# Kernel tuning notes

Measured on AMD Instinct MI355X. Metric: run time of the kernel, lower is better.

Reference implementation:

```python
import jax, jax.numpy as jnp
import numpy as np

TEMP1, TEMP2, TEMP3 = 4.0, 5.0, 10.0  # forward() default temps
EPS = 1e-8


def setup_inputs() -> dict:
    key = jax.random.key(0)
    k1, k2 = jax.random.split(key)
    B, L, D = 64, 64, 512
    return {
        "ecg_embs": jax.random.normal(k1, (B, L, D), dtype=jnp.float32),
        "sent_embs": jax.random.normal(k2, (B, L, D), dtype=jnp.float32),
    }


def reference(ecg_embs, sent_embs):
    # Fully-batched version of the original per-sample Python loop.
    # i indexes the sentence (query) sample, j the ecg (context) sample.
    B, L, D = ecg_embs.shape
    # scores[i,j,s,q] = <ecg[j,s,:], sent[i,q,:]>  == contextT @ query in torch
    scores = jnp.einsum('jsd,iqd->ijsq', ecg_embs, sent_embs)
    # 1st softmax over query axis q
    attn = jax.nn.softmax(scores, axis=-1)
    # transpose to (i,j,q,s), temperature-scale, 2nd softmax over source axis s
    attn = jax.nn.softmax(TEMP1 * jnp.swapaxes(attn, -1, -2), axis=-1)  # (i,j,q,s)
    # weightedContext[i,j,q,:] = sum_s attn[i,j,q,s] * ecg[j,s,:]
    wctx = jnp.einsum('ijqs,jsd->ijqd', attn, ecg_embs)
    sent = sent_embs[:, None]  # (i,1,q,d) broadcast over j
    w12 = jnp.sum(sent * wctx, axis=-1)
    w1 = jnp.linalg.norm(sent, axis=-1)
    w2 = jnp.linalg.norm(wctx, axis=-1)
    cos = w12 / jnp.maximum(w1 * w2, EPS)  # (i,j,q)
    # row_sim.mul_(temp2).exp_().sum(dim=1).log() ; similarities[j,i] (cat along dim=1)
    sim = TEMP3 * jnp.log(jnp.sum(jnp.exp(TEMP2 * cos), axis=-1)).T  # (j,i)
    labels = jnp.arange(B)
    logp0 = jax.nn.log_softmax(sim, axis=-1)
    logp1 = jax.nn.log_softmax(sim.T, axis=-1)
    loss0 = -jnp.mean(logp0[labels, labels])
    loss1 = -jnp.mean(logp1[labels, labels])
    # att_maps: list of attn[i] from iteration i == diagonal (i==j) attention,
    # each shaped (1, queryL, ih=1, iw=sourceL); stacked -> (B, 1, L, 1, L)
    att_maps = attn[labels, labels][:, None, :, None, :]
    return (loss0 + loss1) / 2.0, att_maps
```

## Files before the change

### kernel.cpp

```cpp
#include <hip/hip_runtime.h>
#include <math.h>

typedef __attribute__((ext_vector_type(8))) short short8;
typedef __attribute__((ext_vector_type(4))) float f32x4;
typedef __attribute__((ext_vector_type(16))) float f32x16;
typedef unsigned int uint;
typedef unsigned short ushort;

#define T1 4.0f
#define T2 5.0f
#define T3 10.0f
#define EPSF 1e-8f
#define SST 68

__device__ inline ushort f2bf(float x) {
    union { float f; uint u; } a; a.f = x;
    uint r = a.u + 0x7FFFu + ((a.u >> 16) & 1u);
    return (ushort)(r >> 16);
}
__device__ inline float bf2f(ushort h) {
    union { uint u; float f; } a; a.u = ((uint)h) << 16;
    return a.f;
}

#define GLDS(gsrc, ldst) \
    __builtin_amdgcn_global_load_lds( \
        (const __attribute__((address_space(1))) uint*)(gsrc), \
        (__attribute__((address_space(3))) uint*)(ldst), 16, 0, 0)

__global__ __launch_bounds__(256) void prep_kernel(
        const float* __restrict__ ecg, const float* __restrict__ sent,
        char* __restrict__ EH, char* __restrict__ EL,
        char* __restrict__ SH, char* __restrict__ SL,
        char* __restrict__ Gp, float* __restrict__ w1) {
    __shared__ float partial[256];
    const int bid = blockIdx.x;
    const int tensor = bid >> 6, idx = bid & 63;
    const float* src = (tensor ? sent : ecg) + (size_t)idx * 32768;
    char* dh = (tensor ? SH : EH) + (size_t)idx * 65536;
    char* dl = (tensor ? SL : EL) + (size_t)idx * 65536;
    const int tid = threadIdx.x;
    const int r = tid & 63;
    float s2 = 0.f;
    #pragma unroll
    for (int it = 0; it < 4; it++) {
        int kc = it * 4 + (tid >> 6);
        const float* p = src + r * 512 + kc * 32;
        char* oh = dh + kc * 4096 + r * 64;
        char* ol = dl + kc * 4096 + r * 64;
        #pragma unroll
        for (int c = 0; c < 4; c++) {
            float4 v0 = *(const float4*)(p + c * 8);
            float4 v1 = *(const float4*)(p + c * 8 + 4);
            float x[8] = {v0.x, v0.y, v0.z, v0.w, v1.x, v1.y, v1.z, v1.w};
            uint hw[4], lw[4];
            #pragma unroll
            for (int e = 0; e < 4; e++) {
                float a0 = x[2 * e], a1 = x[2 * e + 1];
                ushort h0 = f2bf(a0), h1 = f2bf(a1);
                hw[e] = (uint)h0 | ((uint)h1 << 16);
                ushort l0 = f2bf(a0 - bf2f(h0)), l1 = f2bf(a1 - bf2f(h1));
                lw[e] = (uint)l0 | ((uint)l1 << 16);
                s2 += a0 * a0 + a1 * a1;
            }
            int phys = (c + (r >> 1)) & 3;
            uint4 H; H.x = hw[0]; H.y = hw[1]; H.z = hw[2]; H.w = hw[3];
            *(uint4*)(oh + phys * 16) = H;
            uint4 L; L.x = lw[0]; L.y = lw[1]; L.z = lw[2]; L.w = lw[3];
            *(uint4*)(ol + phys * 16) = L;
        }
    }
    partial[tid] = s2;
    __syncthreads();
    if (tensor == 1) {
        if (tid < 64) {
            float t = partial[tid] + partial[tid + 64] + partial[tid + 128] + partial[tid + 192];
            w1[idx * 64 + tid] = sqrtf(t);
        }
        return;
    }

    {
        const char* srcH = EH + (size_t)idx * 65536;
        const char* srcL = EL + (size_t)idx * 65536;
        const int wv = tid >> 6, lane = tid & 63;
        const int wq = wv >> 1, wn = wv & 1;
        const int quad = lane >> 4, ln = lane & 15;

        int ao[2], bo[2];
        #pragma unroll
        for (int mi = 0; mi < 2; mi++) {
            int R = 32 * wq + 16 * mi + ln;
            ao[mi] = R * 64 + ((quad + (R >> 1)) & 3) * 16;
        }
        #pragma unroll
        for (int ni = 0; ni < 2; ni++) {
            int R = 32 * wn + 16 * ni + ln;
            bo[ni] = R * 64 + ((quad + (R >> 1)) & 3) * 16;
        }

        f32x4 acc[2][2];
        #pragma unroll
        for (int a = 0; a < 2; a++)
            #pragma unroll
            for (int b = 0; b < 2; b++) acc[a][b] = (f32x4){0.f, 0.f, 0.f, 0.f};

        #pragma unroll 2
        for (int kc = 0; kc < 16; kc++) {
            const char* ph = srcH + (size_t)kc * 4096;
            const char* pl = srcL + (size_t)kc * 4096;
            short8 ah[2], al[2], bh[2], bl[2];
            #pragma unroll
            for (int mi = 0; mi < 2; mi++) {
                ah[mi] = *(const short8*)(ph + ao[mi]);
                al[mi] = *(const short8*)(pl + ao[mi]);
            }
            #pragma unroll
            for (int ni = 0; ni < 2; ni++) {
                bh[ni] = *(const short8*)(ph + bo[ni]);
                bl[ni] = *(const short8*)(pl + bo[ni]);
            }
            #pragma unroll
            for (int mi = 0; mi < 2; mi++)
                #pragma unroll
                for (int ni = 0; ni < 2; ni++) {
                    acc[mi][ni] = __builtin_amdgcn_mfma_f32_16x16x32_bf16(ah[mi], bh[ni], acc[mi][ni], 0, 0, 0);
                    acc[mi][ni] = __builtin_amdgcn_mfma_f32_16x16x32_bf16(ah[mi], bl[ni], acc[mi][ni], 0, 0, 0);
                    acc[mi][ni] = __builtin_amdgcn_mfma_f32_16x16x32_bf16(al[mi], bh[ni], acc[mi][ni], 0, 0, 0);
                }
        }
        #pragma unroll
        for (int mi = 0; mi < 2; mi++)
            #pragma unroll
            for (int ni = 0; ni < 2; ni++)
                #pragma unroll
                for (int rr = 0; rr < 4; rr++) {
                    int t = 32 * wq + 16 * mi + quad * 4 + rr;
                    int u = 32 * wn + 16 * ni + ln;
                    float g = acc[mi][ni][rr];
                    ushort h = f2bf(g);
                    ushort l = f2bf(g - bf2f(h));
                    char* base = Gp + (size_t)idx * 16384 + t * 128 + (((u >> 3) + t) & 7) * 16 + (u & 7) * 2;
                    *(ushort*)base = h;
                    *(ushort*)(base + 8192) = l;
                }
    }
}

__global__ __launch_bounds__(256, 4) void pair_kernel(
        const char* __restrict__ EH, const char* __restrict__ EL,
        const char* __restrict__ SH, const char* __restrict__ SL,
        const char* __restrict__ Gp, const float* __restrict__ w1g,
        float* __restrict__ simval, float* __restrict__ out) {

    __shared__ __align__(16) char lds[33792];
    __shared__ __align__(16) float mz[64];
    __shared__ float w12all[256], w2all[256];

    const int tid = threadIdx.x;
    const int bn = blockIdx.x;
    const int xcd = bn & 7, slot = bn >> 3;
    const int T = xcd * 8 + (slot >> 4);
    const int wp = slot & 15;
    const int bi = (T >> 3) * 4 + (wp >> 2);
    const int bj = (T & 7) * 4 + (wp & 3);
    const int i0 = bi * 2, j0 = bj * 2;

    const int wv = tid >> 6, lane = tid & 63;
    const int wq = wv >> 1, wn = wv & 1;
    const int l5 = lane >> 5, l31 = lane & 31;

    int aoff[2][2], boff[2][2];
    #pragma unroll
    for (int ti = 0; ti < 2; ti++)
        #pragma unroll
        for (int kh = 0; kh < 2; kh++) {
            int cc = l5 + 2 * kh;
            int Ra = 64 * ti + 32 * wq + l31;
            aoff[ti][kh] = Ra * 64 + ((cc + (Ra >> 1)) & 3) * 16;
            int Rb = 64 * ti + 32 * wn + l31;
            boff[ti][kh] = 16384 + Rb * 64 + ((cc + (Rb >> 1)) & 3) * 16;
        }

    const char* gA; const char* gB; int ldoff;
    if (wv == 0)      { gA = EH + (size_t)j0 * 65536;       gB = EH + (size_t)(j0 + 1) * 65536; ldoff = 0; }
    else if (wv == 1) { gA = EL + (size_t)j0 * 65536;       gB = EL + (size_t)(j0 + 1) * 65536; ldoff = 8192; }
    else if (wv == 2) { gA = SH + (size_t)i0 * 65536;       gB = SH + (size_t)(i0 + 1) * 65536; ldoff = 16384; }
    else              { gA = SL + (size_t)i0 * 65536;       gB = SL + (size_t)(i0 + 1) * 65536; ldoff = 24576; }
    gA += lane * 16; gB += lane * 16;

    const f32x16 zf = {0.f,0.f,0.f,0.f,0.f,0.f,0.f,0.f,0.f,0.f,0.f,0.f,0.f,0.f,0.f,0.f};
    f32x16 acc[2][2];
    acc[0][0] = zf; acc[0][1] = zf; acc[1][0] = zf; acc[1][1] = zf;

    for (int kc = 0; kc < 16; kc++) {
        #pragma unroll
        for (int n = 0; n < 4; n++) GLDS(gA + n * 1024, lds + ldoff + n * 1024);
        #pragma unroll
        for (int n = 0; n < 4; n++) GLDS(gB + n * 1024, lds + ldoff + 4096 + n * 1024);
        gA += 4096; gB += 4096;
        __syncthreads();
        short8 bh[2][2], bl[2][2];
        #pragma unroll
        for (int ni = 0; ni < 2; ni++)
            #pragma unroll
            for (int kh = 0; kh < 2; kh++) {
                bh[ni][kh] = *(const short8*)(lds + boff[ni][kh]);
                bl[ni][kh] = *(const short8*)(lds + boff[ni][kh] + 8192);
            }
        #pragma unroll
        for (int mi = 0; mi < 2; mi++) {
            short8 ah[2], al[2];
            #pragma unroll
            for (int kh = 0; kh < 2; kh++) {
                ah[kh] = *(const short8*)(lds + aoff[mi][kh]);
                al[kh] = *(const short8*)(lds + aoff[mi][kh] + 8192);
            }
            #pragma unroll
            for (int ni = 0; ni < 2; ni++)
                #pragma unroll
                for (int kh = 0; kh < 2; kh++) {
                    acc[mi][ni] = __builtin_amdgcn_mfma_f32_32x32x16_bf16(ah[kh], bh[ni][kh], acc[mi][ni], 0, 0, 0);
                    acc[mi][ni] = __builtin_amdgcn_mfma_f32_32x32x16_bf16(ah[kh], bl[ni][kh], acc[mi][ni], 0, 0, 0);
                    acc[mi][ni] = __builtin_amdgcn_mfma_f32_32x32x16_bf16(al[kh], bh[ni][kh], acc[mi][ni], 0, 0, 0);
                }
        }
        __syncthreads();
    }

    float* SsT = (float*)lds;
    float* yQ  = (float*)lds;
    char*  Pb  = lds + 17408;

    #pragma unroll
    for (int pr = 0; pr < 4; pr++) {
        const int a = pr >> 1, b = pr & 1;
        const int i = i0 + b, j = j0 + a;

        {
            f32x16 v = acc[a][b];
            int q = 32 * wn + l31;
            #pragma unroll
            for (int g = 0; g < 4; g++) {
                int s0 = 32 * wq + 4 * l5 + 8 * g;
                *(f32x4*)(SsT + q * SST + s0) =
                    (f32x4){v[4 * g], v[4 * g + 1], v[4 * g + 2], v[4 * g + 3]};
            }
        }
        __syncthreads();

        {
            const int s = tid >> 2, c = tid & 3;
            float vv[16]; float m = -1e30f;
            #pragma unroll
            for (int t = 0; t < 16; t++) {
                int tt = (t + 4 * c) & 15;
                vv[t] = SsT[(16 * c + tt) * SST + s];
                m = fmaxf(m, vv[t]);
            }
            m = fmaxf(m, __shfl_xor(m, 1));
            m = fmaxf(m, __shfl_xor(m, 2));
            float sum = 0.f;
            #pragma unroll
            for (int t = 0; t < 16; t++) sum += __expf(vv[t] - m);
            sum += __shfl_xor(sum, 1);
            sum += __shfl_xor(sum, 2);
            if (c == 0) mz[s] = m + __logf(sum);
        }
        __syncthreads();

        {
            const int q = tid >> 2, c = tid & 3;
            float sc[16], at[16];
            #pragma unroll
            for (int r4 = 0; r4 < 4; r4++)
                *(f32x4*)(sc + 4 * r4) = *(const f32x4*)(SsT + q * SST + 16 * c + 4 * r4);
            float mzv[16];
            #pragma unroll
            for (int r4 = 0; r4 < 4; r4++)
                *(f32x4*)(mzv + 4 * r4) = *(const f32x4*)(mz + 16 * c + 4 * r4);
            float m2 = -1e30f;
            #pragma unroll
            for (int t = 0; t < 16; t++) {
                at[t] = __expf(sc[t] - mzv[t]);
                m2 = fmaxf(m2, T1 * at[t]);
            }
            m2 = fmaxf(m2, __shfl_xor(m2, 1));
            m2 = fmaxf(m2, __shfl_xor(m2, 2));
            float sum = 0.f;
            #pragma unroll
            for (int t = 0; t < 16; t++) { at[t] = __expf(T1 * at[t] - m2); sum += at[t]; }
            sum += __shfl_xor(sum, 1);
            sum += __shfl_xor(sum, 2);
            float inv = 1.f / sum;
            float p12 = 0.f;
            #pragma unroll
            for (int t = 0; t < 16; t++) { at[t] *= inv; p12 += at[t] * sc[t]; }
            p12 += __shfl_xor(p12, 1);
            p12 += __shfl_xor(p12, 2);
            if (c == 0) w12all[pr * 64 + q] = p12;

            if (i == j) {
                float* om = out + 1 + (size_t)i * 4096;
                #pragma unroll
                for (int t = 0; t < 16; t++) om[q * 64 + c * 16 + t] = at[t];
            }

            uint hw[8], lw[8];
            #pragma unroll
            for (int e = 0; e < 8; e++) {
                ushort h0 = f2bf(at[2 * e]), h1 = f2bf(at[2 * e + 1]);
                hw[e] = (uint)h0 | ((uint)h1 << 16);
                ushort l0 = f2bf(at[2 * e] - bf2f(h0)), l1 = f2bf(at[2 * e + 1] - bf2f(h1));
                lw[e] = (uint)l0 | ((uint)l1 << 16);
            }
            int p0 = (2 * c + q) & 7, p1 = (2 * c + 1 + q) & 7;
            uint4 W;
            W.x = hw[0]; W.y = hw[1]; W.z = hw[2]; W.w = hw[3];
            *(uint4*)(Pb + q * 128 + p0 * 16) = W;
            W.x = hw[4]; W.y = hw[5]; W.z = hw[6]; W.w = hw[7];
            *(uint4*)(Pb + q * 128 + p1 * 16) = W;
            W.x = lw[0]; W.y = lw[1]; W.z = lw[2]; W.w = lw[3];
            *(uint4*)(Pb + 8192 + q * 128 + p0 * 16) = W;
            W.x = lw[4]; W.y = lw[5]; W.z = lw[6]; W.w = lw[7];
            *(uint4*)(Pb + 8192 + q * 128 + p1 * 16) = W;
        }
        __syncthreads();

        f32x16 acc2 = zf;
        {
            const char* Gq = Gp + (size_t)j * 16384;
            const int u = 32 * wn + l31;
            const int q = 32 * wq + l31;
            short8 gh[4], gl[4];
            #pragma unroll
            for (int ks = 0; ks < 4; ks++) {
                int cc = l5 + 2 * ks;
                int phg = (cc + u) & 7;
                gh[ks] = *(const short8*)(Gq + u * 128 + phg * 16);
                gl[ks] = *(const short8*)(Gq + 8192 + u * 128 + phg * 16);
            }
            #pragma unroll
            for (int ks = 0; ks < 4; ks++) {
                int cc = l5 + 2 * ks;
                int php = (cc + q) & 7;
                short8 pah = *(const short8*)(Pb + q * 128 + php * 16);
                short8 pal = *(const short8*)(Pb + 8192 + q * 128 + php * 16);
                acc2 = __builtin_amdgcn_mfma_f32_32x32x16_bf16(pah, gh[ks], acc2, 0, 0, 0);
                acc2 = __builtin_amdgcn_mfma_f32_32x32x16_bf16(pah, gl[ks], acc2, 0, 0, 0);
                acc2 = __builtin_amdgcn_mfma_f32_32x32x16_bf16(pal, gh[ks], acc2, 0, 0, 0);
            }
        }

        {
            const int u = 32 * wn + l31;
            #pragma unroll
            for (int g = 0; g < 4; g++) {
                int qb = 32 * wq + 4 * l5 + 8 * g;
                yQ[(qb + 0) * SST + u] = acc2[4 * g + 0];
                yQ[(qb + 1) * SST + u] = acc2[4 * g + 1];
                yQ[(qb + 2) * SST + u] = acc2[4 * g + 2];
                yQ[(qb + 3) * SST + u] = acc2[4 * g + 3];
            }
        }
        __syncthreads();

        {
            const int q = tid >> 2, c = tid & 3;
            int p0 = (2 * c + q) & 7, p1 = (2 * c + 1 + q) & 7;
            uint4 H0 = *(const uint4*)(Pb + q * 128 + p0 * 16);
            uint4 H1 = *(const uint4*)(Pb + q * 128 + p1 * 16);
            uint4 L0 = *(const uint4*)(Pb + 8192 + q * 128 + p0 * 16);
            uint4 L1 = *(const uint4*)(Pb + 8192 + q * 128 + p1 * 16);
            uint hw[8] = {H0.x,H0.y,H0.z,H0.w, H1.x,H1.y,H1.z,H1.w};
            uint lw[8] = {L0.x,L0.y,L0.z,L0.w, L1.x,L1.y,L1.z,L1.w};
            float vy[16];
            #pragma unroll
            for (int r4 = 0; r4 < 4; r4++)
                *(f32x4*)(vy + 4 * r4) = *(const f32x4*)(yQ + q * SST + 16 * c + 4 * r4);
            float s = 0.f;
            #pragma unroll
            for (int e = 0; e < 8; e++) {
                float q0v = bf2f((ushort)(hw[e] & 0xFFFFu)) + bf2f((ushort)(lw[e] & 0xFFFFu));
                float q1v = bf2f((ushort)(hw[e] >> 16))     + bf2f((ushort)(lw[e] >> 16));
                s += q0v * vy[2 * e];
                s += q1v * vy[2 * e + 1];
            }
            s += __shfl_xor(s, 1);
            s += __shfl_xor(s, 2);
            if (c == 0) w2all[pr * 64 + q] = s;
        }
        __syncthreads();
    }

    {
        const int pr = wv;
        const int ii = i0 + (pr & 1), jj = j0 + (pr >> 1);
        float w2 = sqrtf(fmaxf(w2all[pr * 64 + lane], 0.f));
        float cosv = w12all[pr * 64 + lane] / fmaxf(w1g[ii * 64 + lane] * w2, EPSF);
        float e = __expf(T2 * cosv);
        #pragma unroll
        for (int off = 32; off; off >>= 1) e += __shfl_down(e, off);
        if (lane == 0) simval[ii * 64 + jj] = T3 * __logf(e);
    }
}

__global__ __launch_bounds__(256) void loss_kernel(const float* __restrict__ val,
                                                   float* __restrict__ out) {
    __shared__ float v[4096];
    const int tid = threadIdx.x;
    #pragma unroll
    for (int k = 0; k < 4; k++)
        ((float4*)v)[tid + k * 256] = ((const float4*)val)[tid + k * 256];
    __syncthreads();
    if (tid < 64) {
        int i = tid;
        float rmax = -1e30f, cmax = -1e30f;
        for (int jj = 0; jj < 64; jj++) {
            rmax = fmaxf(rmax, v[i * 64 + jj]);
            cmax = fmaxf(cmax, v[jj * 64 + i]);
        }
        float rs = 0.f, cs = 0.f;
        for (int jj = 0; jj < 64; jj++) {
            rs += __expf(v[i * 64 + jj] - rmax);
            cs += __expf(v[jj * 64 + i] - cmax);
        }
        float rlse = rmax + __logf(rs);
        float clse = cmax + __logf(cs);
        float part = 2.f * v[i * 64 + i] - rlse - clse;
        #pragma unroll
        for (int off = 32; off; off >>= 1) part += __shfl_down(part, off);
        if (i == 0) out[0] = -part / 128.f;
    }
}

extern "C" void kernel_launch(void* const* d_in, const int* in_sizes, int n_in,
                              void* d_out, int out_size, void* d_ws, size_t ws_size,
                              hipStream_t stream) {
    (void)in_sizes; (void)n_in; (void)out_size; (void)ws_size;
    const float* ecg  = (const float*)d_in[0];
    const float* sent = (const float*)d_in[1];
    float* out = (float*)d_out;

    char* ws = (char*)d_ws;
    float* w1v  = (float*)ws;
    float* simv = (float*)(ws + 16384);
    char* EH = ws + 32768;
    char* EL = EH + (size_t)64 * 65536;
    char* SH = EL + (size_t)64 * 65536;
    char* SL = SH + (size_t)64 * 65536;
    char* Gp = SL + (size_t)64 * 65536;

    prep_kernel <<<128, 256, 0, stream>>>(ecg, sent, EH, EL, SH, SL, Gp, w1v);
    pair_kernel <<<1024, 256, 0, stream>>>(EH, EL, SH, SL, Gp, w1v, simv, out);
    loss_kernel <<<1,   256, 0, stream>>>(simv, out);
}
```

Baseline: 156.1 us.

## Double-buffer the score GEMM global-to-LDS loads and stage G matrix through LDS

The main scores GEMM loop now uses two LDS buffers, prefetching the next K-chunk with direct global-to-LDS loads while MFMAs run on the current one. This halves the barriers per iteration and rearranges the LDS fragment layout so each lane reads contiguous 32-byte rows. The second GEMM now stages the G matrix into LDS with cooperative loads instead of each wave reading scattered global fragments. The cost is extra barriers in the epilogue, and the G staging may overwrite LDS regions that other stages still use.

```diff
diff --git a/kernel.cpp b/kernel.cpp
--- a/kernel.cpp
+++ b/kernel.cpp
@@ -170,61 +170,63 @@
     const int wq = wv >> 1, wn = wv & 1;
     const int l5 = lane >> 5, l31 = lane & 31;
 
-    int aoff[2][2], boff[2][2];
-    #pragma unroll
-    for (int ti = 0; ti < 2; ti++)
-        #pragma unroll
-        for (int kh = 0; kh < 2; kh++) {
-            int cc = l5 + 2 * kh;
-            int Ra = 64 * ti + 32 * wq + l31;
-            aoff[ti][kh] = Ra * 64 + ((cc + (Ra >> 1)) & 3) * 16;
-            int Rb = 64 * ti + 32 * wn + l31;
-            boff[ti][kh] = 16384 + Rb * 64 + ((cc + (Rb >> 1)) & 3) * 16;
-        }
-
-    const char* gA; const char* gB; int ldoff;
-    if (wv == 0)      { gA = EH + (size_t)j0 * 65536;       gB = EH + (size_t)(j0 + 1) * 65536; ldoff = 0; }
-    else if (wv == 1) { gA = EL + (size_t)j0 * 65536;       gB = EL + (size_t)(j0 + 1) * 65536; ldoff = 8192; }
-    else if (wv == 2) { gA = SH + (size_t)i0 * 65536;       gB = SH + (size_t)(i0 + 1) * 65536; ldoff = 16384; }
-    else              { gA = SL + (size_t)i0 * 65536;       gB = SL + (size_t)(i0 + 1) * 65536; ldoff = 24576; }
-    gA += lane * 16; gB += lane * 16;
+    const int laneoff = (lane >> 1) * 64;
+    const int ph0 = (((lane & 1) + (lane >> 2)) & 3) * 16;
+    const int ph1 = (((lane & 1) + (lane >> 2) + 2) & 3) * 16;
+
+    const char* gA; const char* gB;
+    if (wv == 0)      { gA = EH + (size_t)j0 * 65536; gB = EH + (size_t)(j0 + 1) * 65536; }
+    else if (wv == 1) { gA = EL + (size_t)j0 * 65536; gB = EL + (size_t)(j0 + 1) * 65536; }
+    else if (wv == 2) { gA = SH + (size_t)i0 * 65536; gB = SH + (size_t)(i0 + 1) * 65536; }
+    else              { gA = SL + (size_t)i0 * 65536; gB = SL + (size_t)(i0 + 1) * 65536; }
+
+    const int fr = l31 * 32 + l5 * 16;
+    const int fa = wq * 1024 + fr;
+    const int fb = wn * 1024 + fr;
 
     const f32x16 zf = {0.f,0.f,0.f,0.f,0.f,0.f,0.f,0.f,0.f,0.f,0.f,0.f,0.f,0.f,0.f,0.f};
     f32x16 acc[2][2];
     acc[0][0] = zf; acc[0][1] = zf; acc[1][0] = zf; acc[1][1] = zf;
 
-    for (int kc = 0; kc < 16; kc++) {
-        #pragma unroll
-        for (int n = 0; n < 4; n++) GLDS(gA + n * 1024, lds + ldoff + n * 1024);
-        #pragma unroll
-        for (int n = 0; n < 4; n++) GLDS(gB + n * 1024, lds + ldoff + 4096 + n * 1024);
-        gA += 4096; gB += 4096;
-        __syncthreads();
-        short8 bh[2][2], bl[2][2];
-        #pragma unroll
-        for (int ni = 0; ni < 2; ni++)
-            #pragma unroll
-            for (int kh = 0; kh < 2; kh++) {
-                bh[ni][kh] = *(const short8*)(lds + boff[ni][kh]);
-                bl[ni][kh] = *(const short8*)(lds + boff[ni][kh] + 8192);
-            }
-        #pragma unroll
-        for (int mi = 0; mi < 2; mi++) {
-            short8 ah[2], al[2];
-            #pragma unroll
-            for (int kh = 0; kh < 2; kh++) {
-                ah[kh] = *(const short8*)(lds + aoff[mi][kh]);
-                al[kh] = *(const short8*)(lds + aoff[mi][kh] + 8192);
-            }
-            #pragma unroll
-            for (int ni = 0; ni < 2; ni++)
-                #pragma unroll
-                for (int kh = 0; kh < 2; kh++) {
-                    acc[mi][ni] = __builtin_amdgcn_mfma_f32_32x32x16_bf16(ah[kh], bh[ni][kh], acc[mi][ni], 0, 0, 0);
-                    acc[mi][ni] = __builtin_amdgcn_mfma_f32_32x32x16_bf16(ah[kh], bl[ni][kh], acc[mi][ni], 0, 0, 0);
-                    acc[mi][ni] = __builtin_amdgcn_mfma_f32_32x32x16_bf16(al[kh], bh[ni][kh], acc[mi][ni], 0, 0, 0);
-                }
-        }
+    {
+        char* d = lds + wv * 4096;
+        GLDS(gA + laneoff + ph0,        d);
+        GLDS(gA + 2048 + laneoff + ph0, d + 1024);
+        GLDS(gB + laneoff + ph0,        d + 2048);
+        GLDS(gB + 2048 + laneoff + ph0, d + 3072);
+    }
+    __syncthreads();
+
+    #pragma unroll 2
+    for (int it = 0; it < 32; ++it) {
+        if (it < 31) {
+            const int it2 = it + 1;
+            const char* sA = gA + (size_t)(it2 >> 1) * 4096;
+            const char* sB = gB + (size_t)(it2 >> 1) * 4096;
+            const int ph = (it2 & 1) ? ph1 : ph0;
+            char* d = lds + (it2 & 1) * 16384 + wv * 4096;
+            GLDS(sA + laneoff + ph,        d);
+            GLDS(sA + 2048 + laneoff + ph, d + 1024);
+            GLDS(sB + laneoff + ph,        d + 2048);
+            GLDS(sB + 2048 + laneoff + ph, d + 3072);
+        }
+        const char* L = lds + (it & 1) * 16384;
+        short8 ah[2], al[2], bh[2], bl[2];
+        #pragma unroll
+        for (int x = 0; x < 2; x++) {
+            ah[x] = *(const short8*)(L + x * 2048 + fa);
+            al[x] = *(const short8*)(L + 4096 + x * 2048 + fa);
+            bh[x] = *(const short8*)(L + 8192 + x * 2048 + fb);
+            bl[x] = *(const short8*)(L + 12288 + x * 2048 + fb);
+        }
+        #pragma unroll
+        for (int mi = 0; mi < 2; mi++)
+            #pragma unroll
+            for (int ni = 0; ni < 2; ni++) {
+                acc[mi][ni] = __builtin_amdgcn_mfma_f32_32x32x16_bf16(ah[mi], bh[ni], acc[mi][ni], 0, 0, 0);
+                acc[mi][ni] = __builtin_amdgcn_mfma_f32_32x32x16_bf16(ah[mi], bl[ni], acc[mi][ni], 0, 0, 0);
+                acc[mi][ni] = __builtin_amdgcn_mfma_f32_32x32x16_bf16(al[mi], bh[ni], acc[mi][ni], 0, 0, 0);
+            }
         __syncthreads();
     }
 
@@ -327,30 +329,35 @@
         }
         __syncthreads();
 
+        {
+            const char* gs = Gp + (size_t)j * 16384 + wv * 4096 + lane * 16;
+            char* gd = lds + wv * 4096;
+            GLDS(gs,        gd);
+            GLDS(gs + 1024, gd + 1024);
+            GLDS(gs + 2048, gd + 2048);
+            GLDS(gs + 3072, gd + 3072);
+        }
+        __syncthreads();
+
         f32x16 acc2 = zf;
         {
-            const char* Gq = Gp + (size_t)j * 16384;
             const int u = 32 * wn + l31;
             const int q = 32 * wq + l31;
-            short8 gh[4], gl[4];
-            #pragma unroll
-            for (int ks = 0; ks < 4; ks++) {
-                int cc = l5 + 2 * ks;
-                int phg = (cc + u) & 7;
-                gh[ks] = *(const short8*)(Gq + u * 128 + phg * 16);
-                gl[ks] = *(const short8*)(Gq + 8192 + u * 128 + phg * 16);
-            }
             #pragma unroll
             for (int ks = 0; ks < 4; ks++) {
                 int cc = l5 + 2 * ks;
                 int php = (cc + q) & 7;
+                int phg = (cc + u) & 7;
                 short8 pah = *(const short8*)(Pb + q * 128 + php * 16);
                 short8 pal = *(const short8*)(Pb + 8192 + q * 128 + php * 16);
-                acc2 = __builtin_amdgcn_mfma_f32_32x32x16_bf16(pah, gh[ks], acc2, 0, 0, 0);
-                acc2 = __builtin_amdgcn_mfma_f32_32x32x16_bf16(pah, gl[ks], acc2, 0, 0, 0);
-                acc2 = __builtin_amdgcn_mfma_f32_32x32x16_bf16(pal, gh[ks], acc2, 0, 0, 0);
-            }
-        }
+                short8 gbh = *(const short8*)(lds + u * 128 + phg * 16);
+                short8 gbl = *(const short8*)(lds + 8192 + u * 128 + phg * 16);
+                acc2 = __builtin_amdgcn_mfma_f32_32x32x16_bf16(pah, gbh, acc2, 0, 0, 0);
+                acc2 = __builtin_amdgcn_mfma_f32_32x32x16_bf16(pah, gbl, acc2, 0, 0, 0);
+                acc2 = __builtin_amdgcn_mfma_f32_32x32x16_bf16(pal, gbh, acc2, 0, 0, 0);
+            }
+        }
+        __syncthreads();
 
         {
             const int u = 32 * wn + l31;
```

After: 159.1 us. No clear change (+2.0%).
